# Optimization experiments

Hardware: AMD Instinct MI355X
Metric: run time of the kernel (lower is better)

Reference implementation:

```python
import jax
import jax.numpy as jnp
import numpy as np
from jax import lax

NUM_TAGS = 24
BATCH = 8192
SEQ_LEN = 512


def setup_inputs() -> dict:
    key = jax.random.key(0)
    k1, k2 = jax.random.split(key)
    inputs = jax.random.normal(k1, (BATCH, SEQ_LEN, NUM_TAGS), dtype=jnp.float32)
    # glorot_uniform for (num_tags, num_tags)
    limit = float(np.sqrt(6.0 / (NUM_TAGS + NUM_TAGS)))
    transitions = jax.random.uniform(
        k2, (NUM_TAGS, NUM_TAGS), dtype=jnp.float32, minval=-limit, maxval=limit
    )
    return {"inputs": inputs, "transitions": transitions}


def _viterbi_decode(potentials, transitions):
    """Linear-chain CRF Viterbi decode (full-length sequences).

    potentials: [B, T, K] unary scores; transitions: [K, K] (prev -> cur).
    Returns int32 tag sequence [B, T].
    """
    emissions = jnp.swapaxes(potentials, 0, 1)  # [T, B, K]

    def fwd(alpha, emit_t):
        # scores[b, i, j] = alpha[b, i] + transitions[i, j]
        scores = alpha[:, :, None] + transitions[None, :, :]  # [B, K, K]
        bp = jnp.argmax(scores, axis=1).astype(jnp.int32)      # [B, K] best prev tag
        alpha_new = jnp.max(scores, axis=1) + emit_t            # [B, K]
        return alpha_new, bp

    alpha_T, bps = lax.scan(fwd, emissions[0], emissions[1:])  # bps: [T-1, B, K]
    last_tag = jnp.argmax(alpha_T, axis=-1).astype(jnp.int32)  # [B]

    def bwd(tag_next, bp_t):
        # bp_t[b, tag_next[b]] = best tag at step t given tag at t+1
        tag_t = jnp.take_along_axis(bp_t, tag_next[:, None], axis=1)[:, 0]
        return tag_t, tag_t

    _, tags_prefix = lax.scan(bwd, last_tag, bps, reverse=True)  # [T-1, B]
    tags = jnp.concatenate([tags_prefix, last_tag[None, :]], axis=0)  # [T, B]
    return jnp.swapaxes(tags, 0, 1)  # [B, T]


def reference(inputs, transitions):
    # Inference path of CRF.call: Viterbi decode then one-hot encode.
    viterbi = _viterbi_decode(inputs, transitions)            # [B, T] int32
    return jax.nn.one_hot(viterbi, NUM_TAGS, dtype=inputs.dtype)  # [B, T, K]
```

## Files before the change

### kernel.cpp

```cpp
#include <hip/hip_runtime.h>
#include <stdint.h>

#define B 8192
#define T 512
#define K 24

__device__ __forceinline__ float max3f(float a, float b, float c) {
    return fmaxf(fmaxf(a, b), c);
}

__global__ __launch_bounds__(64) __attribute__((amdgpu_waves_per_eu(1, 1)))
void crf_forward(const float* __restrict__ inp,
                 const float* __restrict__ trans,
                 float* __restrict__ out)
{
    __shared__ float alpha[2][8][K];

    const int lane = threadIdx.x;
    const int g    = lane >> 3;
    const int l    = lane & 7;
    const int c0   = 3 * l;
    const int b    = blockIdx.x * 8 + g;

    float tc[3][K];
#pragma unroll
    for (int j = 0; j < 3; ++j)
#pragma unroll
        for (int i = 0; i < K; ++i) tc[j][i] = trans[i * K + c0 + j];

    const float* ebl = inp + (size_t)b * T * K + c0;
    float*       obl = out + (size_t)b * T * K + c0;

    float* a0 = &alpha[0][g][0];
    float* a1 = &alpha[1][g][0];

    {
        float x0 = ebl[0], x1 = ebl[1], x2 = ebl[2];
        a0[c0] = x0; a0[c0 + 1] = x1; a0[c0 + 2] = x2;
        obl[0] = x0; obl[1] = x1; obl[2] = x2;
    }

    float eA0 = ebl[1*K],   eA1 = ebl[1*K+1],   eA2 = ebl[1*K+2];
    float eB0 = ebl[2*K],   eB1 = ebl[2*K+1],   eB2 = ebl[2*K+2];
    float eC0 = ebl[3*K],   eC1 = ebl[3*K+1],   eC2 = ebl[3*K+2];
    float eD0 = ebl[4*K],   eD1 = ebl[4*K+1],   eD2 = ebl[4*K+2];

#define STEP(AC, AN, E0, E1, E2, TT) do {                                     \
    float a_[K];                                                              \
    _Pragma("unroll")                                                         \
    for (int c = 0; c < 6; ++c) {                                             \
        float4 v_ = ((const float4*)(AC))[c];                                 \
        a_[4*c] = v_.x; a_[4*c+1] = v_.y; a_[4*c+2] = v_.z; a_[4*c+3] = v_.w; \
    }                                                                         \
    float r_[3];                                                              \
    _Pragma("unroll")                                                         \
    for (int j = 0; j < 3; ++j) {                                             \
        float u_[8];                                                          \
        _Pragma("unroll")                                                     \
        for (int k = 0; k < 8; ++k)                                           \
            u_[k] = max3f(a_[3*k]   + tc[j][3*k],                             \
                          a_[3*k+1] + tc[j][3*k+1],                           \
                          a_[3*k+2] + tc[j][3*k+2]);                          \
        float w0_ = max3f(u_[0], u_[1], u_[2]);                               \
        float w1_ = max3f(u_[3], u_[4], u_[5]);                               \
        float w2_ = fmaxf(u_[6], u_[7]);                                      \
        r_[j] = max3f(w0_, w1_, w2_);                                         \
    }                                                                         \
    float o0_ = r_[0] + (E0), o1_ = r_[1] + (E1), o2_ = r_[2] + (E2);         \
    (AN)[c0] = o0_; (AN)[c0+1] = o1_; (AN)[c0+2] = o2_;                       \
    float* gp_ = obl + (size_t)(TT) * K;                                      \
    gp_[0] = o0_; gp_[1] = o1_; gp_[2] = o2_;                                 \
} while (0)

#pragma unroll 1
    for (int ch = 0; ch < 127; ++ch) {
        const int t = 1 + 4 * ch;
        const float* p4 = ebl + (size_t)(t + 4) * K;
        const float* p5 = ebl + (size_t)(t + 5) * K;
        const float* p6 = ebl + (size_t)(t + 6) * K;
        int t7 = t + 7; t7 = t7 > 511 ? 511 : t7;
        const float* p7 = ebl + (size_t)t7 * K;
        float nA0 = p4[0], nA1 = p4[1], nA2 = p4[2];
        float nB0 = p5[0], nB1 = p5[1], nB2 = p5[2];
        float nC0 = p6[0], nC1 = p6[1], nC2 = p6[2];
        float nD0 = p7[0], nD1 = p7[1], nD2 = p7[2];

        STEP(a0, a1, eA0, eA1, eA2, t);
        STEP(a1, a0, eB0, eB1, eB2, t + 1);
        STEP(a0, a1, eC0, eC1, eC2, t + 2);
        STEP(a1, a0, eD0, eD1, eD2, t + 3);

        eA0 = nA0; eA1 = nA1; eA2 = nA2;
        eB0 = nB0; eB1 = nB1; eB2 = nB2;
        eC0 = nC0; eC1 = nC1; eC2 = nC2;
        eD0 = nD0; eD1 = nD1; eD2 = nD2;
    }
    STEP(a0, a1, eA0, eA1, eA2, 509);
    STEP(a1, a0, eB0, eB1, eB2, 510);
    STEP(a0, a1, eC0, eC1, eC2, 511);
#undef STEP
}

__device__ __forceinline__ float groupmax32(float v) {
    float t;
    t = __int_as_float(__builtin_amdgcn_mov_dpp(__float_as_int(v), 0xB1, 0xF, 0xF, true));
    v = fmaxf(v, t);
    t = __int_as_float(__builtin_amdgcn_mov_dpp(__float_as_int(v), 0x4E, 0xF, 0xF, true));
    v = fmaxf(v, t);
    t = __int_as_float(__builtin_amdgcn_mov_dpp(__float_as_int(v), 0x141, 0xF, 0xF, true));
    v = fmaxf(v, t);
    t = __int_as_float(__builtin_amdgcn_mov_dpp(__float_as_int(v), 0x140, 0xF, 0xF, true));
    v = fmaxf(v, t);
    t = __int_as_float(__builtin_amdgcn_ds_swizzle(__float_as_int(v), 0x401F));
    v = fmaxf(v, t);
    return v;
}

__global__ __launch_bounds__(256) __attribute__((amdgpu_waves_per_eu(4, 4)))
void crf_backtrack(const float* __restrict__ trans,
                   float* __restrict__ out)
{
    __shared__ float tl[K * 25];

    const int tid = threadIdx.x;
    for (int idx = tid; idx < K * K; idx += 256) {
        int i = idx / K, j = idx - K * i;
        tl[i * 25 + j] = trans[idx];
    }
    __syncthreads();

    const int lane = tid & 63;
    const int half = lane >> 5;
    const int i    = lane & 31;
    const int wv   = tid >> 6;
    const int b    = blockIdx.x * 8 + wv * 2 + half;
    const int shmt = half * 32;

    const bool act = (i < K);
    const int  io  = act ? i : (K - 1);

    float* ob = out + (size_t)b * T * K;
    const float* rp  = ob + (size_t)511 * K + io;
    float*       wpp = ob + (size_t)511 * K + io;

    float q[8];
#pragma unroll
    for (int s = 0; s < 8; ++s) { q[7 - s] = *rp; rp -= K; }

    int cur;
    {
        float s = act ? q[7] : -INFINITY;
        float M = groupmax32(s);
        uint32_t m32 = (uint32_t)(__ballot(s == M) >> shmt);
        cur = (int)__builtin_ctz(m32);
        if (act) *wpp = (i == cur) ? 1.0f : 0.0f;
        wpp -= K;
        q[7] = *rp; rp -= K;
    }

#define STEP_BT(S, TT) do {                                                   \
    float tv_ = tl[io * 25 + cur];                                            \
    float s_  = act ? (q[S] + tv_) : -INFINITY;                               \
    float M_  = groupmax32(s_);                                               \
    uint32_t m32_ = (uint32_t)(__ballot(s_ == M_) >> shmt);                   \
    cur = (int)__builtin_ctz(m32_);                                           \
    if (act) *wpp = (i == cur) ? 1.0f : 0.0f;                                 \
    wpp -= K;                                                                 \
    if ((TT) >= 8) { q[S] = *rp; rp -= K; }                                   \
} while (0)

#pragma unroll 1
    for (int it = 0; it < 63; ++it) {
        const int t0 = 510 - 8 * it;
        STEP_BT(6, t0);     STEP_BT(5, t0 - 1);
        STEP_BT(4, t0 - 2); STEP_BT(3, t0 - 3);
        STEP_BT(2, t0 - 4); STEP_BT(1, t0 - 5);
        STEP_BT(0, t0 - 6); STEP_BT(7, t0 - 7);
    }
    STEP_BT(6, 6); STEP_BT(5, 5); STEP_BT(4, 4);
    STEP_BT(3, 3); STEP_BT(2, 2); STEP_BT(1, 1); STEP_BT(0, 0);
#undef STEP_BT
}

extern "C" void kernel_launch(void* const* d_in, const int* in_sizes, int n_in,
                              void* d_out, int out_size, void* d_ws, size_t ws_size,
                              hipStream_t stream) {
    const float* inp   = (const float*)d_in[0];
    const float* trans = (const float*)d_in[1];
    float*       out   = (float*)d_out;

    crf_forward<<<B / 8, 64, 0, stream>>>(inp, trans, out);
    crf_backtrack<<<B / 8, 256, 0, stream>>>(trans, out);
}
```

Before: 344.0 us.

## Split forward CRF recursion over 12 lanes per sequence with float2 I/O

The forward Viterbi kernel now gives each sequence 16 lanes, 12 of them active with 2 tags each, instead of 8 lanes with 3 tags each. A wave therefore handles 4 sequences rather than 8, and the grid doubles. Emission loads and alpha stores become float2 vector accesses, and occupancy is raised to 2 waves per EU. The aim is to shorten the serial per-step max-plus chain at the cost of idle lanes (4 of 16 per group) and more waves overall.

```diff
diff --git a/kernel.cpp b/kernel.cpp
--- a/kernel.cpp
+++ b/kernel.cpp
@@ -9,52 +9,55 @@
     return fmaxf(fmaxf(a, b), c);
 }
 
-__global__ __launch_bounds__(64) __attribute__((amdgpu_waves_per_eu(1, 1)))
+__global__ __launch_bounds__(64) __attribute__((amdgpu_waves_per_eu(2, 2)))
 void crf_forward(const float* __restrict__ inp,
                  const float* __restrict__ trans,
                  float* __restrict__ out)
 {
-    __shared__ float alpha[2][8][K];
+    __shared__ float alpha[2][4][K];
 
     const int lane = threadIdx.x;
-    const int g    = lane >> 3;
-    const int l    = lane & 7;
-    const int c0   = 3 * l;
-    const int b    = blockIdx.x * 8 + g;
+    const int grp  = lane >> 4;
+    const int l    = lane & 15;
+    const bool act = (l < 12);
+    const int c0   = act ? 2 * l : 22;
+    const int b    = blockIdx.x * 4 + grp;
 
-    float tc[3][K];
+    float tc[2][K];
 #pragma unroll
-    for (int j = 0; j < 3; ++j)
+    for (int j = 0; j < 2; ++j)
 #pragma unroll
         for (int i = 0; i < K; ++i) tc[j][i] = trans[i * K + c0 + j];
 
     const float* ebl = inp + (size_t)b * T * K + c0;
     float*       obl = out + (size_t)b * T * K + c0;
 
-    float* a0 = &alpha[0][g][0];
-    float* a1 = &alpha[1][g][0];
+    float* a0 = &alpha[0][grp][0];
+    float* a1 = &alpha[1][grp][0];
 
     {
-        float x0 = ebl[0], x1 = ebl[1], x2 = ebl[2];
-        a0[c0] = x0; a0[c0 + 1] = x1; a0[c0 + 2] = x2;
-        obl[0] = x0; obl[1] = x1; obl[2] = x2;
+        float2 x = *(const float2*)(ebl);
+        if (act) {
+            a0[c0] = x.x; a0[c0 + 1] = x.y;
+            *(float2*)(obl) = x;
+        }
     }
 
-    float eA0 = ebl[1*K],   eA1 = ebl[1*K+1],   eA2 = ebl[1*K+2];
-    float eB0 = ebl[2*K],   eB1 = ebl[2*K+1],   eB2 = ebl[2*K+2];
-    float eC0 = ebl[3*K],   eC1 = ebl[3*K+1],   eC2 = ebl[3*K+2];
-    float eD0 = ebl[4*K],   eD1 = ebl[4*K+1],   eD2 = ebl[4*K+2];
+    float2 eA = *(const float2*)(ebl + 1 * K);
+    float2 eB = *(const float2*)(ebl + 2 * K);
+    float2 eC = *(const float2*)(ebl + 3 * K);
+    float2 eD = *(const float2*)(ebl + 4 * K);
 
-#define STEP(AC, AN, E0, E1, E2, TT) do {                                     \
+#define STEP(AC, AN, E, TT) do {                                              \
     float a_[K];                                                              \
     _Pragma("unroll")                                                         \
     for (int c = 0; c < 6; ++c) {                                             \
         float4 v_ = ((const float4*)(AC))[c];                                 \
         a_[4*c] = v_.x; a_[4*c+1] = v_.y; a_[4*c+2] = v_.z; a_[4*c+3] = v_.w; \
     }                                                                         \
-    float r_[3];                                                              \
+    float r_[2];                                                              \
     _Pragma("unroll")                                                         \
-    for (int j = 0; j < 3; ++j) {                                             \
+    for (int j = 0; j < 2; ++j) {                                             \
         float u_[8];                                                          \
         _Pragma("unroll")                                                     \
         for (int k = 0; k < 8; ++k)                                           \
@@ -66,38 +69,33 @@
         float w2_ = fmaxf(u_[6], u_[7]);                                      \
         r_[j] = max3f(w0_, w1_, w2_);                                         \
     }                                                                         \
-    float o0_ = r_[0] + (E0), o1_ = r_[1] + (E1), o2_ = r_[2] + (E2);         \
-    (AN)[c0] = o0_; (AN)[c0+1] = o1_; (AN)[c0+2] = o2_;                       \
-    float* gp_ = obl + (size_t)(TT) * K;                                      \
-    gp_[0] = o0_; gp_[1] = o1_; gp_[2] = o2_;                                 \
+    float o0_ = r_[0] + (E).x, o1_ = r_[1] + (E).y;                           \
+    if (act) {                                                                \
+        (AN)[c0] = o0_; (AN)[c0 + 1] = o1_;                                   \
+        float2 st_; st_.x = o0_; st_.y = o1_;                                 \
+        *(float2*)(obl + (size_t)(TT) * K) = st_;                             \
+    }                                                                         \
 } while (0)
 
 #pragma unroll 1
     for (int ch = 0; ch < 127; ++ch) {
         const int t = 1 + 4 * ch;
-        const float* p4 = ebl + (size_t)(t + 4) * K;
-        const float* p5 = ebl + (size_t)(t + 5) * K;
-        const float* p6 = ebl + (size_t)(t + 6) * K;
+        float2 nA = *(const float2*)(ebl + (size_t)(t + 4) * K);
+        float2 nB = *(const float2*)(ebl + (size_t)(t + 5) * K);
+        float2 nC = *(const float2*)(ebl + (size_t)(t + 6) * K);
         int t7 = t + 7; t7 = t7 > 511 ? 511 : t7;
-        const float* p7 = ebl + (size_t)t7 * K;
-        float nA0 = p4[0], nA1 = p4[1], nA2 = p4[2];
-        float nB0 = p5[0], nB1 = p5[1], nB2 = p5[2];
-        float nC0 = p6[0], nC1 = p6[1], nC2 = p6[2];
-        float nD0 = p7[0], nD1 = p7[1], nD2 = p7[2];
+        float2 nD = *(const float2*)(ebl + (size_t)t7 * K);
 
-        STEP(a0, a1, eA0, eA1, eA2, t);
-        STEP(a1, a0, eB0, eB1, eB2, t + 1);
-        STEP(a0, a1, eC0, eC1, eC2, t + 2);
-        STEP(a1, a0, eD0, eD1, eD2, t + 3);
+        STEP(a0, a1, eA, t);
+        STEP(a1, a0, eB, t + 1);
+        STEP(a0, a1, eC, t + 2);
+        STEP(a1, a0, eD, t + 3);
 
-        eA0 = nA0; eA1 = nA1; eA2 = nA2;
-        eB0 = nB0; eB1 = nB1; eB2 = nB2;
-        eC0 = nC0; eC1 = nC1; eC2 = nC2;
-        eD0 = nD0; eD1 = nD1; eD2 = nD2;
+        eA = nA; eB = nB; eC = nC; eD = nD;
     }
-    STEP(a0, a1, eA0, eA1, eA2, 509);
-    STEP(a1, a0, eB0, eB1, eB2, 510);
-    STEP(a0, a1, eC0, eC1, eC2, 511);
+    STEP(a0, a1, eA, 509);
+    STEP(a1, a0, eB, 510);
+    STEP(a0, a1, eC, 511);
 #undef STEP
 }
 
@@ -189,6 +187,6 @@
     const float* trans = (const float*)d_in[1];
     float*       out   = (float*)d_out;
 
-    crf_forward<<<B / 8, 64, 0, stream>>>(inp, trans, out);
+    crf_forward<<<B / 4, 64, 0, stream>>>(inp, trans, out);
     crf_backtrack<<<B / 8, 256, 0, stream>>>(trans, out);
 }
```

After: 352.8 us. +2.5%, slower.

## Exchange forward alpha via DPP and swizzle instead of LDS

Applied to the files above, without the earlier changes.

The forward Viterbi recurrence no longer writes alpha to shared memory and reads it back each step. Each lane's three alpha values are spread across the 8-lane group with ds_swizzle (xor 4) and DPP lane shuffles (xor 2, xor 1). The transition registers are permuted at load time so each gathered slot lines up with the right source tag. This takes the LDS store, wait and load round trip off the serial dependency chain, in exchange for 21 cross-lane ops per step. One of those ops, ds_swizzle, still goes through the LDS hardware path.

```diff
diff --git a/kernel.cpp b/kernel.cpp
--- a/kernel.cpp
+++ b/kernel.cpp
@@ -14,62 +14,83 @@
                  const float* __restrict__ trans,
                  float* __restrict__ out)
 {
-    __shared__ float alpha[2][8][K];
-
     const int lane = threadIdx.x;
     const int g    = lane >> 3;
     const int l    = lane & 7;
     const int c0   = 3 * l;
     const int b    = blockIdx.x * 8 + g;
 
-    float tc[3][K];
+    const int X[8] = {0, 4, 2, 6, 1, 5, 3, 7};
+    float tcr[3][K];
 #pragma unroll
     for (int j = 0; j < 3; ++j)
 #pragma unroll
-        for (int i = 0; i < K; ++i) tc[j][i] = trans[i * K + c0 + j];
+        for (int k = 0; k < 8; ++k) {
+            const int rl = 3 * (l ^ X[k]);
+#pragma unroll
+            for (int c = 0; c < 3; ++c)
+                tcr[j][3 * k + c] = trans[(rl + c) * K + c0 + j];
+        }
 
     const float* ebl = inp + (size_t)b * T * K + c0;
     float*       obl = out + (size_t)b * T * K + c0;
 
-    float* a0 = &alpha[0][g][0];
-    float* a1 = &alpha[1][g][0];
-
+    float n0, n1, n2;
     {
-        float x0 = ebl[0], x1 = ebl[1], x2 = ebl[2];
-        a0[c0] = x0; a0[c0 + 1] = x1; a0[c0 + 2] = x2;
-        obl[0] = x0; obl[1] = x1; obl[2] = x2;
-    }
-
-    float eA0 = ebl[1*K],   eA1 = ebl[1*K+1],   eA2 = ebl[1*K+2];
-    float eB0 = ebl[2*K],   eB1 = ebl[2*K+1],   eB2 = ebl[2*K+2];
-    float eC0 = ebl[3*K],   eC1 = ebl[3*K+1],   eC2 = ebl[3*K+2];
-    float eD0 = ebl[4*K],   eD1 = ebl[4*K+1],   eD2 = ebl[4*K+2];
-
-#define STEP(AC, AN, E0, E1, E2, TT) do {                                     \
-    float a_[K];                                                              \
-    _Pragma("unroll")                                                         \
-    for (int c = 0; c < 6; ++c) {                                             \
-        float4 v_ = ((const float4*)(AC))[c];                                 \
-        a_[4*c] = v_.x; a_[4*c+1] = v_.y; a_[4*c+2] = v_.z; a_[4*c+3] = v_.w; \
-    }                                                                         \
+        n0 = ebl[0]; n1 = ebl[1]; n2 = ebl[2];
+        obl[0] = n0; obl[1] = n1; obl[2] = n2;
+    }
+
+    float eA0 = ebl[1*K], eA1 = ebl[1*K+1], eA2 = ebl[1*K+2];
+    float eB0 = ebl[2*K], eB1 = ebl[2*K+1], eB2 = ebl[2*K+2];
+    float eC0 = ebl[3*K], eC1 = ebl[3*K+1], eC2 = ebl[3*K+2];
+    float eD0 = ebl[4*K], eD1 = ebl[4*K+1], eD2 = ebl[4*K+2];
+
+#define XG(v) __builtin_amdgcn_ds_swizzle((v), 0x101F)
+#define D2(v) __builtin_amdgcn_mov_dpp((v), 0x4E, 0xF, 0xF, true)
+#define D1(v) __builtin_amdgcn_mov_dpp((v), 0xB1, 0xF, 0xF, true)
+
+#define STEP(E0, E1, E2, TT) do {                                             \
+    const int i0_ = __float_as_int(n0);                                       \
+    const int i1_ = __float_as_int(n1);                                       \
+    const int i2_ = __float_as_int(n2);                                       \
+    const int b0_ = XG(i0_), b1_ = XG(i1_), b2_ = XG(i2_);                    \
+    const int q0_ = D2(i0_), q1_ = D2(i1_), q2_ = D2(i2_);                    \
+    const int q3_ = D2(b0_), q4_ = D2(b1_), q5_ = D2(b2_);                    \
+    const int d0_ = D1(i0_), d1_ = D1(i1_), d2_  = D1(i2_);                   \
+    const int d3_ = D1(b0_), d4_ = D1(b1_), d5_  = D1(b2_);                   \
+    const int d6_ = D1(q0_), d7_ = D1(q1_), d8_  = D1(q2_);                   \
+    const int d9_ = D1(q3_), d10_ = D1(q4_), d11_ = D1(q5_);                  \
+    float s_[K];                                                              \
+    s_[0]  = n0;                    s_[1]  = n1;                              \
+    s_[2]  = n2;                    s_[3]  = __int_as_float(b0_);             \
+    s_[4]  = __int_as_float(b1_);   s_[5]  = __int_as_float(b2_);             \
+    s_[6]  = __int_as_float(q0_);   s_[7]  = __int_as_float(q1_);             \
+    s_[8]  = __int_as_float(q2_);   s_[9]  = __int_as_float(q3_);             \
+    s_[10] = __int_as_float(q4_);   s_[11] = __int_as_float(q5_);             \
+    s_[12] = __int_as_float(d0_);   s_[13] = __int_as_float(d1_);             \
+    s_[14] = __int_as_float(d2_);   s_[15] = __int_as_float(d3_);             \
+    s_[16] = __int_as_float(d4_);   s_[17] = __int_as_float(d5_);             \
+    s_[18] = __int_as_float(d6_);   s_[19] = __int_as_float(d7_);             \
+    s_[20] = __int_as_float(d8_);   s_[21] = __int_as_float(d9_);             \
+    s_[22] = __int_as_float(d10_);  s_[23] = __int_as_float(d11_);            \
     float r_[3];                                                              \
     _Pragma("unroll")                                                         \
     for (int j = 0; j < 3; ++j) {                                             \
         float u_[8];                                                          \
         _Pragma("unroll")                                                     \
         for (int k = 0; k < 8; ++k)                                           \
-            u_[k] = max3f(a_[3*k]   + tc[j][3*k],                             \
-                          a_[3*k+1] + tc[j][3*k+1],                           \
-                          a_[3*k+2] + tc[j][3*k+2]);                          \
+            u_[k] = max3f(s_[3*k]   + tcr[j][3*k],                            \
+                          s_[3*k+1] + tcr[j][3*k+1],                          \
+                          s_[3*k+2] + tcr[j][3*k+2]);                         \
         float w0_ = max3f(u_[0], u_[1], u_[2]);                               \
         float w1_ = max3f(u_[3], u_[4], u_[5]);                               \
         float w2_ = fmaxf(u_[6], u_[7]);                                      \
         r_[j] = max3f(w0_, w1_, w2_);                                         \
     }                                                                         \
-    float o0_ = r_[0] + (E0), o1_ = r_[1] + (E1), o2_ = r_[2] + (E2);         \
-    (AN)[c0] = o0_; (AN)[c0+1] = o1_; (AN)[c0+2] = o2_;                       \
+    n0 = r_[0] + (E0); n1 = r_[1] + (E1); n2 = r_[2] + (E2);                  \
     float* gp_ = obl + (size_t)(TT) * K;                                      \
-    gp_[0] = o0_; gp_[1] = o1_; gp_[2] = o2_;                                 \
+    gp_[0] = n0; gp_[1] = n1; gp_[2] = n2;                                    \
 } while (0)
 
 #pragma unroll 1
@@ -85,20 +106,23 @@
         float nC0 = p6[0], nC1 = p6[1], nC2 = p6[2];
         float nD0 = p7[0], nD1 = p7[1], nD2 = p7[2];
 
-        STEP(a0, a1, eA0, eA1, eA2, t);
-        STEP(a1, a0, eB0, eB1, eB2, t + 1);
-        STEP(a0, a1, eC0, eC1, eC2, t + 2);
-        STEP(a1, a0, eD0, eD1, eD2, t + 3);
+        STEP(eA0, eA1, eA2, t);
+        STEP(eB0, eB1, eB2, t + 1);
+        STEP(eC0, eC1, eC2, t + 2);
+        STEP(eD0, eD1, eD2, t + 3);
 
         eA0 = nA0; eA1 = nA1; eA2 = nA2;
         eB0 = nB0; eB1 = nB1; eB2 = nB2;
         eC0 = nC0; eC1 = nC1; eC2 = nC2;
         eD0 = nD0; eD1 = nD1; eD2 = nD2;
     }
-    STEP(a0, a1, eA0, eA1, eA2, 509);
-    STEP(a1, a0, eB0, eB1, eB2, 510);
-    STEP(a0, a1, eC0, eC1, eC2, 511);
+    STEP(eA0, eA1, eA2, 509);
+    STEP(eB0, eB1, eB2, 510);
+    STEP(eC0, eC1, eC2, 511);
 #undef STEP
+#undef XG
+#undef D2
+#undef D1
 }
 
 __device__ __forceinline__ float groupmax32(float v) {
```

After: 337.7 us (median of 2 runs). No clear change (-1.8%).
